# Performance work log

Hardware: AMD Instinct MI355X
Metric: run time of the kernel (lower is better)

The kernel has to match this reference:

```python
import jax, jax.numpy as jnp
import numpy as np

EMBED = 512
QDIM = 512
VDIM = 512
SRC = 4096
BSZ = 64


def setup_inputs() -> dict:
    key = jax.random.key(0)
    ks = jax.random.split(key, 6)
    query = jax.random.normal(ks[0], (BSZ, QDIM), dtype=jnp.float32)
    value = jax.random.normal(ks[1], (SRC, BSZ, VDIM), dtype=jnp.float32)
    key_padding_mask = jnp.zeros((SRC, BSZ), dtype=bool)
    # params: torch init uniform(-0.1, 0.1); b=0, g=sqrt(1/embed)
    Wq = jax.random.uniform(ks[2], (EMBED, QDIM), minval=-0.1, maxval=0.1, dtype=jnp.float32)
    Wv = jax.random.uniform(ks[3], (EMBED, VDIM), minval=-0.1, maxval=0.1, dtype=jnp.float32)
    v = jax.random.uniform(ks[4], (EMBED,), minval=-0.1, maxval=0.1, dtype=jnp.float32)
    b = jnp.zeros((EMBED,), dtype=jnp.float32)
    g = jnp.full((1,), np.sqrt(1.0 / EMBED), dtype=jnp.float32)
    return {"query": query, "value": value, "key_padding_mask": key_padding_mask,
            "Wq": Wq, "Wv": Wv, "v": v, "b": b, "g": g}


def reference(query, value, key_padding_mask, Wq, Wv, v, b, g):
    # projected_query: [1, bsz, embed]; key: [src, bsz, embed]
    pq = (query @ Wq.T)[None, :, :]
    key = jnp.einsum('sbv,ev->sbe', value, Wv)
    normed_v = g * v / jnp.linalg.norm(v)  # [embed]
    # attn_scores: [src, bsz]
    attn_scores = jnp.einsum('e,sbe->sb', normed_v, jnp.tanh(pq + key + b))
    attn_scores = jnp.where(key_padding_mask, -jnp.inf, attn_scores)
    attn_scores = jax.nn.softmax(attn_scores, axis=0)
    # context: [bsz, value_dim]
    context = jnp.einsum('sb,sbv->bv', attn_scores, value)
    return (context, attn_scores, attn_scores)
```

## Files before the change

### kernel.cpp

```cpp
#include <hip/hip_runtime.h>
#include <hip/hip_bf16.h>
#include <math.h>

typedef __bf16 bf16x8 __attribute__((ext_vector_type(8)));
typedef __bf16 bf16x4 __attribute__((ext_vector_type(4)));
typedef float  f32x4  __attribute__((ext_vector_type(4)));

#define SRC 4096
#define BSZ 64
#define EMB 512

__device__ __forceinline__ float fast_tanh(float x) {
  float ax = fabsf(x);
  float t  = __expf(-2.0f * ax);
  float r  = 1.0f - 2.0f * t / (1.0f + t);
  return copysignf(r, x);
}

__global__ void prep_nv(const float* __restrict__ v, const float* __restrict__ g,
                        float* __restrict__ nv) {
  __shared__ float red[256];
  int t = threadIdx.x;
  float a = v[t], b = v[t + 256];
  red[t] = a * a + b * b;
  __syncthreads();
  for (int o = 128; o > 0; o >>= 1) {
    if (t < o) red[t] += red[t + o];
    __syncthreads();
  }
  float scale = g[0] / sqrtf(red[0]);
  nv[t]       = a * scale;
  nv[t + 256] = b * scale;
}

__global__ void prep_pqb(const float* __restrict__ query, const float* __restrict__ Wq,
                         const float* __restrict__ bias, float* __restrict__ pqb) {
  __shared__ float q[EMB];
  int b = blockIdx.x >> 1, t = threadIdx.x;
  int e = (blockIdx.x & 1) * 256 + t;
  q[t]       = query[b * EMB + t];
  q[t + 256] = query[b * EMB + t + 256];
  __syncthreads();
  const float* wr = Wq + (size_t)e * EMB;
  float a0 = 0.f, a1 = 0.f;
#pragma unroll 8
  for (int k = 0; k < EMB; k += 8) {
    float4 q0 = *reinterpret_cast<const float4*>(&q[k]);
    float4 w0 = *reinterpret_cast<const float4*>(&wr[k]);
    float4 q1 = *reinterpret_cast<const float4*>(&q[k + 4]);
    float4 w1 = *reinterpret_cast<const float4*>(&wr[k + 4]);
    a0 += q0.x * w0.x + q0.y * w0.y + q0.z * w0.z + q0.w * w0.w;
    a1 += q1.x * w1.x + q1.y * w1.y + q1.z * w1.z + q1.w * w1.w;
  }
  pqb[b * EMB + e] = a0 + a1 + bias[e];
}

__global__ void pack_wv(const float* __restrict__ Wv, __bf16* __restrict__ wvpk) {
  int tid  = blockIdx.x * 256 + threadIdx.x;
  int lane = tid & 63;
  int ks   = (tid >> 6) & 15;
  int nsub = tid >> 10;
  int e  = nsub * 16 + (lane & 15);
  int k0 = ks * 32 + (lane >> 4) * 8;
  const float* src = Wv + (size_t)e * EMB + k0;
  bf16x8 o;
#pragma unroll
  for (int j = 0; j < 8; ++j) o[j] = (__bf16)src[j];
  *reinterpret_cast<bf16x8*>(wvpk + (size_t)tid * 8) = o;
}

__global__ __launch_bounds__(512, 4)
void scores_kernel(const float* __restrict__ value, const float* __restrict__ pqb,
                   const float* __restrict__ nv, const __bf16* __restrict__ wvpk,
                   float* __restrict__ scoresT) {
  __shared__ __bf16 As[2][64 * 128];
  __shared__ float red[8][BSZ];
  const int s = blockIdx.x;
  const int t = threadIdx.x;
  const int w  = t >> 6;
  const int l  = t & 63;
  const int lr = l & 15;
  const int lk = l >> 4;

  const int srow = t >> 3;
  const int ssub = t & 7;
  const float* sbase = value + (size_t)s * (BSZ * EMB) + (size_t)srow * EMB + ssub * 4;

  float4 h0[4], h1[4];
  auto issue = [&](int c, float4* h) {
    const float* p = sbase + c * 128;
#pragma unroll
    for (int j = 0; j < 4; ++j) h[j] = *reinterpret_cast<const float4*>(p + j * 32);
  };
  auto write_lds = [&](int buf, const float4* h) {
#pragma unroll
    for (int j = 0; j < 4; ++j) {
      int kg  = (ssub >> 1) + j * 4;
      int kgp = kg ^ (srow & 7);
      bf16x4 o;
      o[0] = (__bf16)h[j].x; o[1] = (__bf16)h[j].y;
      o[2] = (__bf16)h[j].z; o[3] = (__bf16)h[j].w;
      *reinterpret_cast<bf16x4*>(&As[buf][srow * 128 + kgp * 8 + (ssub & 1) * 4]) = o;
    }
  };

  f32x4 acc[4][4];
#pragma unroll
  for (int m = 0; m < 4; ++m)
#pragma unroll
    for (int n = 0; n < 4; ++n)
#pragma unroll
      for (int r = 0; r < 4; ++r) acc[m][n][r] = 0.f;

  auto compute_chunk = [&](int buf, int c) {
#pragma unroll
    for (int ks = 0; ks < 4; ++ks) {
      const int ksg = c * 4 + ks;
      bf16x8 bq[4];
#pragma unroll
      for (int n = 0; n < 4; ++n) {
        int nt = w * 4 + n;
        bq[n] = *reinterpret_cast<const bf16x8*>(
            wvpk + ((size_t)((nt * 16 + ksg) * 64 + l)) * 8);
      }
      const int kgp = ((ks * 4 + lk) ^ (lr & 7)) * 8;
#pragma unroll
      for (int m = 0; m < 4; ++m) {
        bf16x8 a = *reinterpret_cast<const bf16x8*>(&As[buf][(m * 16 + lr) * 128 + kgp]);
#pragma unroll
        for (int n = 0; n < 4; ++n)
          acc[m][n] = __builtin_amdgcn_mfma_f32_16x16x32_bf16(a, bq[n], acc[m][n], 0, 0, 0);
      }
    }
  };

  issue(0, h0);
  issue(1, h1);
  write_lds(0, h0);
  write_lds(1, h1);
  __syncthreads();
  issue(2, h0);
  issue(3, h1);
  compute_chunk(0, 0);
  compute_chunk(1, 1);
  __syncthreads();
  write_lds(0, h0);
  write_lds(1, h1);
  __syncthreads();
  compute_chunk(0, 2);
  compute_chunk(1, 3);

  float sc[16];
#pragma unroll
  for (int i = 0; i < 16; ++i) sc[i] = 0.f;
#pragma unroll
  for (int n = 0; n < 4; ++n) {
    int col = w * 64 + n * 16 + lr;
    float nvc = nv[col];
#pragma unroll
    for (int m = 0; m < 4; ++m) {
#pragma unroll
      for (int r = 0; r < 4; ++r) {
        int brow = m * 16 + lk * 4 + r;
        float x = acc[m][n][r] + pqb[brow * EMB + col];
        sc[m * 4 + r] += nvc * fast_tanh(x);
      }
    }
  }
#pragma unroll
  for (int i = 0; i < 16; ++i) {
    float vsum = sc[i];
#pragma unroll
    for (int off = 1; off < 16; off <<= 1) vsum += __shfl_xor(vsum, off, 64);
    if (lr == 0) red[w][(i >> 2) * 16 + lk * 4 + (i & 3)] = vsum;
  }
  __syncthreads();
  if (t < BSZ) {
    float total = 0.f;
#pragma unroll
    for (int ww = 0; ww < 8; ++ww) total += red[ww][t];
    scoresT[(size_t)t * SRC + s] = total;
  }
}

__global__ void softmax_k(const float* __restrict__ scoresT, const unsigned char* __restrict__ mask,
                          float* __restrict__ pT, float* __restrict__ attn0,
                          float* __restrict__ attn1) {
  __shared__ float buf[SRC];
  __shared__ float red[256];
  int b = blockIdx.x, t = threadIdx.x;
  float mx = -1e30f;
  for (int s = t; s < SRC; s += 256) {
    float x = scoresT[(size_t)b * SRC + s];
    if (mask[(size_t)s * BSZ + b]) x = -1e30f;
    buf[s] = x;
    mx = fmaxf(mx, x);
  }
  red[t] = mx; __syncthreads();
  for (int o = 128; o > 0; o >>= 1) { if (t < o) red[t] = fmaxf(red[t], red[t + o]); __syncthreads(); }
  mx = red[0]; __syncthreads();
  float sum = 0.f;
  for (int s = t; s < SRC; s += 256) { float e = __expf(buf[s] - mx); buf[s] = e; sum += e; }
  red[t] = sum; __syncthreads();
  for (int o = 128; o > 0; o >>= 1) { if (t < o) red[t] += red[t + o]; __syncthreads(); }
  float inv = 1.0f / red[0];
  for (int s = t; s < SRC; s += 256) {
    float p = buf[s] * inv;
    pT[(size_t)b * SRC + s] = p;
    attn0[(size_t)s * BSZ + b] = p;
    attn1[(size_t)s * BSZ + b] = p;
  }
}

__global__ void ctx_partial(const float* __restrict__ value, const float* __restrict__ pT,
                            float* __restrict__ parts) {
  int blk = blockIdx.x;
  int c = blk >> 6;
  int b = blk & 63;
  int t = threadIdx.x;
  const float* pb = pT + (size_t)b * SRC + c * 128;
  float4 acc = make_float4(0.f, 0.f, 0.f, 0.f);
#pragma unroll 8
  for (int i = 0; i < 128; ++i) {
    float p = pb[i];
    float4 vv = *reinterpret_cast<const float4*>(
        value + ((size_t)((c * 128 + i) * BSZ + b)) * EMB + t * 4);
    acc.x += p * vv.x; acc.y += p * vv.y; acc.z += p * vv.z; acc.w += p * vv.w;
  }
  *reinterpret_cast<float4*>(parts + (size_t)blk * EMB + t * 4) = acc;
}

__global__ void ctx_reduce(const float* __restrict__ parts, float* __restrict__ out_ctx) {
  int idx = blockIdx.x * 256 + threadIdx.x;
  float acc = 0.f;
#pragma unroll
  for (int c = 0; c < 32; ++c) acc += parts[(size_t)c * (BSZ * EMB) + idx];
  out_ctx[idx] = acc;
}

extern "C" void kernel_launch(void* const* d_in, const int* in_sizes, int n_in,
                              void* d_out, int out_size, void* d_ws, size_t ws_size,
                              hipStream_t stream) {
  const float* query        = (const float*)d_in[0];
  const float* value        = (const float*)d_in[1];
  const unsigned char* mask = (const unsigned char*)d_in[2];
  const float* Wq           = (const float*)d_in[3];
  const float* Wv           = (const float*)d_in[4];
  const float* v            = (const float*)d_in[5];
  const float* bias         = (const float*)d_in[6];
  const float* g            = (const float*)d_in[7];

  float* out_ctx = (float*)d_out;
  float* attn0   = (float*)d_out + BSZ * EMB;
  float* attn1   = attn0 + SRC * BSZ;

  char* ws = (char*)d_ws;
  float*  nv      = (float*)(ws);
  float*  pqb     = (float*)(ws + 2048);
  __bf16* wvpk    = (__bf16*)(ws + 2048 + 131072);
  float*  scoresT = (float*)(ws + 2048 + 131072 + 524288);
  float*  pT      = scoresT + SRC * BSZ;
  float*  parts   = pT + SRC * BSZ;

  prep_nv<<<1, 256, 0, stream>>>(v, g, nv);
  prep_pqb<<<2 * BSZ, 256, 0, stream>>>(query, Wq, bias, pqb);
  pack_wv<<<128, 256, 0, stream>>>(Wv, wvpk);
  scores_kernel<<<SRC, 512, 0, stream>>>(value, pqb, nv, wvpk, scoresT);
  softmax_k<<<BSZ, 256, 0, stream>>>(scoresT, mask, pT, attn0, attn1);
  ctx_partial<<<BSZ * 32, 128, 0, stream>>>(value, pT, parts);
  ctx_reduce<<<128, 256, 0, stream>>>(parts, out_ctx);
}
```

Measured before the change: 1.030 ms.

## Merge prep kernels, stage full value tile in LDS, cheaper tanh, wider ctx blocks

After: 962.1 us. 6.6% less time.

```diff
diff --git a/kernel.cpp b/kernel.cpp
--- a/kernel.cpp
+++ b/kernel.cpp
@@ -3,106 +3,91 @@
 #include <math.h>
 
 typedef __bf16 bf16x8 __attribute__((ext_vector_type(8)));
-typedef __bf16 bf16x4 __attribute__((ext_vector_type(4)));
 typedef float  f32x4  __attribute__((ext_vector_type(4)));
 
 #define SRC 4096
 #define BSZ 64
 #define EMB 512
 
-__device__ __forceinline__ float fast_tanh(float x) {
-  float ax = fabsf(x);
-  float t  = __expf(-2.0f * ax);
-  float r  = 1.0f - 2.0f * t / (1.0f + t);
-  return copysignf(r, x);
-}
-
-__global__ void prep_nv(const float* __restrict__ v, const float* __restrict__ g,
-                        float* __restrict__ nv) {
+__global__ void prep_all(const float* __restrict__ query, const float* __restrict__ Wq,
+                         const float* __restrict__ bias, const float* __restrict__ v,
+                         const float* __restrict__ g, const float* __restrict__ Wv,
+                         float* __restrict__ nv, float* __restrict__ pqb,
+                         __bf16* __restrict__ wvpk) {
+  __shared__ float sh[EMB];
   __shared__ float red[256];
-  int t = threadIdx.x;
-  float a = v[t], b = v[t + 256];
-  red[t] = a * a + b * b;
-  __syncthreads();
-  for (int o = 128; o > 0; o >>= 1) {
-    if (t < o) red[t] += red[t + o];
+  const int blk = blockIdx.x, t = threadIdx.x;
+  if (blk == 0) {
+    float a = v[t], b = v[t + 256];
+    red[t] = a * a + b * b;
     __syncthreads();
-  }
-  float scale = g[0] / sqrtf(red[0]);
-  nv[t]       = a * scale;
-  nv[t + 256] = b * scale;
-}
-
-__global__ void prep_pqb(const float* __restrict__ query, const float* __restrict__ Wq,
-                         const float* __restrict__ bias, float* __restrict__ pqb) {
-  __shared__ float q[EMB];
-  int b = blockIdx.x >> 1, t = threadIdx.x;
-  int e = (blockIdx.x & 1) * 256 + t;
-  q[t]       = query[b * EMB + t];
-  q[t + 256] = query[b * EMB + t + 256];
-  __syncthreads();
-  const float* wr = Wq + (size_t)e * EMB;
-  float a0 = 0.f, a1 = 0.f;
+    for (int o = 128; o > 0; o >>= 1) {
+      if (t < o) red[t] += red[t + o];
+      __syncthreads();
+    }
+    float scale = g[0] / sqrtf(red[0]);
+    nv[t]       = a * scale;
+    nv[t + 256] = b * scale;
+  } else if (blk <= 128) {
+    int tid  = (blk - 1) * 256 + t;
+    int lane = tid & 63;
+    int ks   = (tid >> 6) & 15;
+    int nsub = tid >> 10;
+    int e  = nsub * 16 + (lane & 15);
+    int k0 = ks * 32 + (lane >> 4) * 8;
+    const float* src = Wv + (size_t)e * EMB + k0;
+    bf16x8 o;
+#pragma unroll
+    for (int j = 0; j < 8; ++j) o[j] = (__bf16)src[j];
+    *reinterpret_cast<bf16x8*>(wvpk + (size_t)tid * 8) = o;
+  } else {
+    int bb = blk - 129;
+    int b = bb >> 1;
+    int e = (bb & 1) * 256 + t;
+    sh[t]       = query[b * EMB + t];
+    sh[t + 256] = query[b * EMB + t + 256];
+    __syncthreads();
+    const float* wr = Wq + (size_t)e * EMB;
+    float a0 = 0.f, a1 = 0.f;
 #pragma unroll 8
-  for (int k = 0; k < EMB; k += 8) {
-    float4 q0 = *reinterpret_cast<const float4*>(&q[k]);
-    float4 w0 = *reinterpret_cast<const float4*>(&wr[k]);
-    float4 q1 = *reinterpret_cast<const float4*>(&q[k + 4]);
-    float4 w1 = *reinterpret_cast<const float4*>(&wr[k + 4]);
-    a0 += q0.x * w0.x + q0.y * w0.y + q0.z * w0.z + q0.w * w0.w;
-    a1 += q1.x * w1.x + q1.y * w1.y + q1.z * w1.z + q1.w * w1.w;
-  }
-  pqb[b * EMB + e] = a0 + a1 + bias[e];
-}
-
-__global__ void pack_wv(const float* __restrict__ Wv, __bf16* __restrict__ wvpk) {
-  int tid  = blockIdx.x * 256 + threadIdx.x;
-  int lane = tid & 63;
-  int ks   = (tid >> 6) & 15;
-  int nsub = tid >> 10;
-  int e  = nsub * 16 + (lane & 15);
-  int k0 = ks * 32 + (lane >> 4) * 8;
-  const float* src = Wv + (size_t)e * EMB + k0;
-  bf16x8 o;
-#pragma unroll
-  for (int j = 0; j < 8; ++j) o[j] = (__bf16)src[j];
-  *reinterpret_cast<bf16x8*>(wvpk + (size_t)tid * 8) = o;
+    for (int k = 0; k < EMB; k += 8) {
+      float4 q0 = *reinterpret_cast<const float4*>(&sh[k]);
+      float4 w0 = *reinterpret_cast<const float4*>(&wr[k]);
+      float4 q1 = *reinterpret_cast<const float4*>(&sh[k + 4]);
+      float4 w1 = *reinterpret_cast<const float4*>(&wr[k + 4]);
+      a0 += q0.x * w0.x + q0.y * w0.y + q0.z * w0.z + q0.w * w0.w;
+      a1 += q1.x * w1.x + q1.y * w1.y + q1.z * w1.z + q1.w * w1.w;
+    }
+    pqb[b * EMB + e] = a0 + a1 + bias[e];
+  }
 }
 
 __global__ __launch_bounds__(512, 4)
 void scores_kernel(const float* __restrict__ value, const float* __restrict__ pqb,
                    const float* __restrict__ nv, const __bf16* __restrict__ wvpk,
                    float* __restrict__ scoresT) {
-  __shared__ __bf16 As[2][64 * 128];
+  __shared__ __bf16 As[BSZ * EMB];
   __shared__ float red[8][BSZ];
   const int s = blockIdx.x;
   const int t = threadIdx.x;
-  const int w  = t >> 6;
-  const int l  = t & 63;
-  const int lr = l & 15;
-  const int lk = l >> 4;
-
-  const int srow = t >> 3;
-  const int ssub = t & 7;
-  const float* sbase = value + (size_t)s * (BSZ * EMB) + (size_t)srow * EMB + ssub * 4;
-
-  float4 h0[4], h1[4];
-  auto issue = [&](int c, float4* h) {
-    const float* p = sbase + c * 128;
-#pragma unroll
-    for (int j = 0; j < 4; ++j) h[j] = *reinterpret_cast<const float4*>(p + j * 32);
-  };
-  auto write_lds = [&](int buf, const float4* h) {
-#pragma unroll
-    for (int j = 0; j < 4; ++j) {
-      int kg  = (ssub >> 1) + j * 4;
-      int kgp = kg ^ (srow & 7);
-      bf16x4 o;
-      o[0] = (__bf16)h[j].x; o[1] = (__bf16)h[j].y;
-      o[2] = (__bf16)h[j].z; o[3] = (__bf16)h[j].w;
-      *reinterpret_cast<bf16x4*>(&As[buf][srow * 128 + kgp * 8 + (ssub & 1) * 4]) = o;
-    }
-  };
+
+  {
+    const int row = t >> 3, sub = t & 7;
+    const float* src = value + (size_t)s * (BSZ * EMB) + (size_t)row * EMB + sub * 8;
+#pragma unroll
+    for (int j = 0; j < 8; ++j) {
+      float4 v0 = *reinterpret_cast<const float4*>(src + j * 64);
+      float4 v1 = *reinterpret_cast<const float4*>(src + j * 64 + 4);
+      int kgp = (sub + j * 8) ^ (row & 7);
+      bf16x8 o;
+      o[0] = (__bf16)v0.x; o[1] = (__bf16)v0.y; o[2] = (__bf16)v0.z; o[3] = (__bf16)v0.w;
+      o[4] = (__bf16)v1.x; o[5] = (__bf16)v1.y; o[6] = (__bf16)v1.z; o[7] = (__bf16)v1.w;
+      *reinterpret_cast<bf16x8*>(&As[row * EMB + kgp * 8]) = o;
+    }
+  }
+  __syncthreads();
+
+  const int w = t >> 6, l = t & 63, lr = l & 15, lk = l >> 4;
 
   f32x4 acc[4][4];
 #pragma unroll
@@ -112,43 +97,29 @@
 #pragma unroll
       for (int r = 0; r < 4; ++r) acc[m][n][r] = 0.f;
 
-  auto compute_chunk = [&](int buf, int c) {
-#pragma unroll
-    for (int ks = 0; ks < 4; ++ks) {
-      const int ksg = c * 4 + ks;
-      bf16x8 bq[4];
-#pragma unroll
-      for (int n = 0; n < 4; ++n) {
-        int nt = w * 4 + n;
-        bq[n] = *reinterpret_cast<const bf16x8*>(
-            wvpk + ((size_t)((nt * 16 + ksg) * 64 + l)) * 8);
-      }
-      const int kgp = ((ks * 4 + lk) ^ (lr & 7)) * 8;
-#pragma unroll
-      for (int m = 0; m < 4; ++m) {
-        bf16x8 a = *reinterpret_cast<const bf16x8*>(&As[buf][(m * 16 + lr) * 128 + kgp]);
-#pragma unroll
-        for (int n = 0; n < 4; ++n)
-          acc[m][n] = __builtin_amdgcn_mfma_f32_16x16x32_bf16(a, bq[n], acc[m][n], 0, 0, 0);
-      }
-    }
-  };
-
-  issue(0, h0);
-  issue(1, h1);
-  write_lds(0, h0);
-  write_lds(1, h1);
-  __syncthreads();
-  issue(2, h0);
-  issue(3, h1);
-  compute_chunk(0, 0);
-  compute_chunk(1, 1);
-  __syncthreads();
-  write_lds(0, h0);
-  write_lds(1, h1);
-  __syncthreads();
-  compute_chunk(0, 2);
-  compute_chunk(1, 3);
+  const __bf16* bp = wvpk + (size_t)(w * 4) * 16 * 512 + (size_t)l * 8;
+  bf16x8 bq[2][4];
+#pragma unroll
+  for (int n = 0; n < 4; ++n)
+    bq[0][n] = *reinterpret_cast<const bf16x8*>(bp + (size_t)(n * 16) * 512);
+
+#pragma unroll
+  for (int ksg = 0; ksg < 16; ++ksg) {
+    if (ksg < 15) {
+#pragma unroll
+      for (int n = 0; n < 4; ++n)
+        bq[(ksg + 1) & 1][n] =
+            *reinterpret_cast<const bf16x8*>(bp + (size_t)(n * 16 + ksg + 1) * 512);
+    }
+    const int kgp = ((ksg * 4 + lk) ^ (lr & 7)) * 8;
+#pragma unroll
+    for (int m = 0; m < 4; ++m) {
+      bf16x8 a = *reinterpret_cast<const bf16x8*>(&As[(m * 16 + lr) * EMB + kgp]);
+#pragma unroll
+      for (int n = 0; n < 4; ++n)
+        acc[m][n] = __builtin_amdgcn_mfma_f32_16x16x32_bf16(a, bq[ksg & 1][n], acc[m][n], 0, 0, 0);
+    }
+  }
 
   float sc[16];
 #pragma unroll
@@ -163,10 +134,13 @@
       for (int r = 0; r < 4; ++r) {
         int brow = m * 16 + lk * 4 + r;
         float x = acc[m][n][r] + pqb[brow * EMB + col];
-        sc[m * 4 + r] += nvc * fast_tanh(x);
+        float e = __expf(2.0f * x);
+        float rcp = __builtin_amdgcn_rcpf(1.0f + e);
+        sc[m * 4 + r] += fmaf(-2.0f * nvc, rcp, nvc);
       }
     }
   }
+
 #pragma unroll
   for (int i = 0; i < 16; ++i) {
     float vsum = sc[i];
@@ -212,22 +186,24 @@
   }
 }
 
-__global__ void ctx_partial(const float* __restrict__ value, const float* __restrict__ pT,
-                            float* __restrict__ parts) {
+__global__ __launch_bounds__(256)
+void ctx_partial(const float* __restrict__ value, const float* __restrict__ pT,
+                 float* __restrict__ parts) {
   int blk = blockIdx.x;
   int c = blk >> 6;
   int b = blk & 63;
   int t = threadIdx.x;
-  const float* pb = pT + (size_t)b * SRC + c * 128;
+  int f4 = t & 127, half = t >> 7;
+  const float* pb = pT + (size_t)b * SRC + c * 256 + half;
+  const float* vb = value + ((size_t)(c * 256 + half) * BSZ + b) * EMB + f4 * 4;
   float4 acc = make_float4(0.f, 0.f, 0.f, 0.f);
 #pragma unroll 8
-  for (int i = 0; i < 128; ++i) {
-    float p = pb[i];
-    float4 vv = *reinterpret_cast<const float4*>(
-        value + ((size_t)((c * 128 + i) * BSZ + b)) * EMB + t * 4);
+  for (int j = 0; j < 128; ++j) {
+    float p = pb[j * 2];
+    float4 vv = *reinterpret_cast<const float4*>(vb + (size_t)j * 2 * BSZ * EMB);
     acc.x += p * vv.x; acc.y += p * vv.y; acc.z += p * vv.z; acc.w += p * vv.w;
   }
-  *reinterpret_cast<float4*>(parts + (size_t)blk * EMB + t * 4) = acc;
+  *reinterpret_cast<float4*>(parts + ((size_t)(c * 2 + half) * BSZ + b) * EMB + f4 * 4) = acc;
 }
 
 __global__ void ctx_reduce(const float* __restrict__ parts, float* __restrict__ out_ctx) {
@@ -262,11 +238,9 @@
   float*  pT      = scoresT + SRC * BSZ;
   float*  parts   = pT + SRC * BSZ;
 
-  prep_nv<<<1, 256, 0, stream>>>(v, g, nv);
-  prep_pqb<<<2 * BSZ, 256, 0, stream>>>(query, Wq, bias, pqb);
-  pack_wv<<<128, 256, 0, stream>>>(Wv, wvpk);
+  prep_all<<<257, 256, 0, stream>>>(query, Wq, bias, v, g, Wv, nv, pqb, wvpk);
   scores_kernel<<<SRC, 512, 0, stream>>>(value, pqb, nv, wvpk, scoresT);
   softmax_k<<<BSZ, 256, 0, stream>>>(scoresT, mask, pT, attn0, attn1);
-  ctx_partial<<<BSZ * 32, 128, 0, stream>>>(value, pT, parts);
+  ctx_partial<<<BSZ * 16, 256, 0, stream>>>(value, pT, parts);
   ctx_reduce<<<128, 256, 0, stream>>>(parts, out_ctx);
 }
```
